# Kernel optimization log

Measured on AMD Instinct MI355X. Metric: run time of the kernel, lower is better.

Reference implementation:

```python
import jax, jax.numpy as jnp
import numpy as np

N = 4096
IN_DIM = 256
OUT_DIM = 256
NUM_HEADS = 4
HEAD_DIM = OUT_DIM // NUM_HEADS


def setup_inputs() -> dict:
    key = jax.random.key(0)
    ks = jax.random.split(key, 10)
    x = jax.random.normal(ks[0], (N, IN_DIM), dtype=jnp.float32)
    adj = jax.random.randint(ks[1], (N, N), 0, 2, dtype=jnp.int32)
    adj = jnp.maximum(adj, jnp.eye(N, dtype=jnp.int32))  # self-loops -> no empty rows
    s_in = 1.0 / np.sqrt(IN_DIM)
    s_out = 1.0 / np.sqrt(OUT_DIM)
    Wq = jax.random.uniform(ks[2], (IN_DIM, OUT_DIM), jnp.float32, -s_in, s_in)
    bq = jnp.zeros((OUT_DIM,), jnp.float32)
    Wk = jax.random.uniform(ks[3], (IN_DIM, OUT_DIM), jnp.float32, -s_in, s_in)
    bk = jnp.zeros((OUT_DIM,), jnp.float32)
    Wv = jax.random.uniform(ks[4], (IN_DIM, OUT_DIM), jnp.float32, -s_in, s_in)
    bv = jnp.zeros((OUT_DIM,), jnp.float32)
    Wo = jax.random.uniform(ks[5], (OUT_DIM, OUT_DIM), jnp.float32, -s_out, s_out)
    bo = jnp.zeros((OUT_DIM,), jnp.float32)
    gamma = jnp.ones((OUT_DIM,), jnp.float32)
    beta = jnp.zeros((OUT_DIM,), jnp.float32)
    return {"x": x, "adj": adj, "Wq": Wq, "bq": bq, "Wk": Wk, "bk": bk,
            "Wv": Wv, "bv": bv, "Wo": Wo, "bo": bo, "gamma": gamma, "beta": beta}


def layer_norm(h, gamma, beta, eps=1e-5):
    mu = jnp.mean(h, axis=-1, keepdims=True)
    var = jnp.mean(jnp.square(h - mu), axis=-1, keepdims=True)
    return (h - mu) * jax.lax.rsqrt(var + eps) * gamma + beta


def reference(x, adj, Wq, bq, Wk, bk, Wv, bv, Wo, bo, gamma, beta):
    n = x.shape[0]
    q_proj = x @ Wq + bq                       # (N, out_dim), reused for residual
    Q = q_proj.reshape(n, NUM_HEADS, HEAD_DIM)
    K = (x @ Wk + bk).reshape(n, NUM_HEADS, HEAD_DIM)
    V = (x @ Wv + bv).reshape(n, NUM_HEADS, HEAD_DIM)
    scores = jnp.einsum('nhd,mhd->nmh', Q, K) / np.sqrt(HEAD_DIM)
    scores = jnp.where(adj[:, :, None] == 0, -jnp.inf, scores)
    attn = jax.nn.softmax(scores, axis=1)      # softmax over neighbor axis m
    out = jnp.einsum('nmh,mhd->nhd', attn, V).reshape(n, OUT_DIM)
    out = out @ Wo + bo
    return layer_norm(out + q_proj, gamma, beta)
```

## Files before the change

### kernel.cpp

```cpp
#include <hip/hip_runtime.h>
#include <math.h>

#define NN 4096
#define DIM 256
#define NHEADS 4
#define HDIM 64

typedef short bf16x8 __attribute__((ext_vector_type(8)));
typedef float f32x4  __attribute__((ext_vector_type(4)));

__device__ __forceinline__ unsigned short f2bf(float f) {
    unsigned int u = __float_as_uint(f);
    u += 0x7fffu + ((u >> 16) & 1u);
    return (unsigned short)(u >> 16);
}
__device__ __forceinline__ float bf2f(unsigned short h) {
    return __uint_as_float(((unsigned int)h) << 16);
}
__device__ __forceinline__ void async16(const void* g, void* l) {
    __builtin_amdgcn_global_load_lds(
        (const __attribute__((address_space(1))) unsigned int*)g,
        (__attribute__((address_space(3))) unsigned int*)l, 16, 0, 0);
}

__global__ __launch_bounds__(256)
void prep_kernel(const float* __restrict__ W0, const float* __restrict__ W1,
                 const float* __restrict__ W2, const float* __restrict__ W3,
                 unsigned short* __restrict__ T0, unsigned short* __restrict__ T1,
                 unsigned short* __restrict__ T2, unsigned short* __restrict__ T3)
{
    __shared__ unsigned short Ts[64][65];
    const int b = blockIdx.x, t = threadIdx.x;
    const int mat = b >> 4, tile = b & 15;
    const int r0 = (tile >> 2) * 64, c0 = (tile & 3) * 64;
    const float* W = (mat == 0) ? W0 : (mat == 1) ? W1 : (mat == 2) ? W2 : W3;
    unsigned short* T = (mat == 0) ? T0 : (mat == 1) ? T1 : (mat == 2) ? T2 : T3;
    {
        int r = t >> 2, c4 = (t & 3) * 16;
        #pragma unroll
        for (int j = 0; j < 4; ++j) {
            float4 v = *reinterpret_cast<const float4*>(W + (size_t)(r0 + r) * DIM + c0 + c4 + j * 4);
            Ts[c4 + j * 4 + 0][r] = f2bf(v.x);
            Ts[c4 + j * 4 + 1][r] = f2bf(v.y);
            Ts[c4 + j * 4 + 2][r] = f2bf(v.z);
            Ts[c4 + j * 4 + 3][r] = f2bf(v.w);
        }
    }
    __syncthreads();
    {
        int d = t >> 2, k4 = (t & 3) * 16;
        #pragma unroll
        for (int j = 0; j < 4; ++j) {
            ushort4 u;
            u.x = Ts[d][k4 + j * 4 + 0];
            u.y = Ts[d][k4 + j * 4 + 1];
            u.z = Ts[d][k4 + j * 4 + 2];
            u.w = Ts[d][k4 + j * 4 + 3];
            *reinterpret_cast<ushort4*>(T + (size_t)(c0 + d) * DIM + r0 + k4 + j * 4) = u;
        }
    }
}

__global__ __launch_bounds__(256)
void qkv_mask(const float* __restrict__ x,
              const unsigned short* __restrict__ WqT, const unsigned short* __restrict__ WkT,
              const unsigned short* __restrict__ WvT,
              const float* __restrict__ bq, const float* __restrict__ bk, const float* __restrict__ bv,
              unsigned short* __restrict__ Qo, unsigned short* __restrict__ Ko,
              unsigned short* __restrict__ VTo,
              const int* __restrict__ adj, unsigned long long* __restrict__ maskT)
{
    const int b = blockIdx.x, t = threadIdx.x, w = t >> 6, l = t & 63;

    if (b >= 384) {
        const int ww = (b - 384) * 4 + w;
        for (int idx = ww; idx < 65536; idx += 8192) {
            const int row = idx >> 4, st = idx & 15;
            const int* ap = adj + (size_t)row * NN + st * 256 + l;
            const int a0 = ap[0];
            const int a1 = ap[64];
            const int a2 = ap[128];
            const int a3 = ap[192];
            unsigned long long b0 = __ballot(a0 != 0);
            unsigned long long b1 = __ballot(a1 != 0);
            unsigned long long b2 = __ballot(a2 != 0);
            unsigned long long b3 = __ballot(a3 != 0);
            if (l < 4) {
                unsigned long long bb = (l == 0) ? b0 : (l == 1) ? b1 : (l == 2) ? b2 : b3;
                maskT[(size_t)row * 64 + st * 4 + l] = bb;
            }
        }
        return;
    }

    const int l15 = l & 15, lg = l >> 4;
    const int which = b >> 7, xb = b & 127;
    const int row0 = xb * 32 + (w >> 1) * 16;
    const int col0 = (w & 1) * 128;
    const unsigned short* WT; const float* bias;
    if (which == 0)      { WT = WqT; bias = bq; }
    else if (which == 1) { WT = WkT; bias = bk; }
    else                 { WT = WvT; bias = bv; }

    f32x4 acc[8] = {};
    for (int k0 = 0; k0 < DIM; k0 += 32) {
        const float* xp = x + (size_t)(row0 + l15) * DIM + k0 + lg * 8;
        float4 x0 = *reinterpret_cast<const float4*>(xp);
        float4 x1 = *reinterpret_cast<const float4*>(xp + 4);
        union { unsigned u[4]; bf16x8 v; } xa;
        asm("v_cvt_pk_bf16_f32 %0, %1, %2" : "=v"(xa.u[0]) : "v"(x0.x), "v"(x0.y));
        asm("v_cvt_pk_bf16_f32 %0, %1, %2" : "=v"(xa.u[1]) : "v"(x0.z), "v"(x0.w));
        asm("v_cvt_pk_bf16_f32 %0, %1, %2" : "=v"(xa.u[2]) : "v"(x1.x), "v"(x1.y));
        asm("v_cvt_pk_bf16_f32 %0, %1, %2" : "=v"(xa.u[3]) : "v"(x1.z), "v"(x1.w));
        #pragma unroll
        for (int nt = 0; nt < 8; ++nt) {
            bf16x8 wb = *(const bf16x8*)(WT + (size_t)(col0 + nt * 16 + l15) * DIM + k0 + lg * 8);
            acc[nt] = __builtin_amdgcn_mfma_f32_16x16x32_bf16(xa.v, wb, acc[nt], 0, 0, 0);
        }
    }
    #pragma unroll
    for (int nt = 0; nt < 8; ++nt) {
        int col = col0 + nt * 16 + l15;
        float bb = bias[col];
        #pragma unroll
        for (int r = 0; r < 4; ++r) {
            int row = row0 + lg * 4 + r;
            float ov = acc[nt][r] + bb;
            if (which == 1) ov *= 0.18033688f;
            unsigned short val = f2bf(ov);
            if (which == 2) {
                int rb = row & 63;
                int vnt = rb >> 4, vlg = (rb >> 2) & 3, vr = rb & 3;
                int pos = ((vnt & 1) << 5) | (vlg << 3) | ((vnt >> 1) << 2) | vr;
                VTo[(size_t)col * NN + ((row & ~63) | pos)] = val;
            } else if (which == 0) Qo[(size_t)row * DIM + col] = val;
            else                   Ko[(size_t)row * DIM + col] = val;
        }
    }
}

template<int NTILES>
__global__ __launch_bounds__(256, 8)
void attn_mfma(const unsigned short* __restrict__ Qb, const unsigned short* __restrict__ Kb,
               const unsigned short* __restrict__ VT, const unsigned long long* __restrict__ maskT,
               unsigned short* __restrict__ Opart, float* __restrict__ lpart)
{
    constexpr int NSTR = NTILES / 4;
    __shared__ unsigned short Kt[2][64][64];
    __shared__ unsigned short Vt[2][64][64];

    const int t = threadIdx.x, w = t >> 6, l = t & 63, l15 = l & 15, lg = l >> 4;
    const int bid = blockIdx.x;
    const int slice = (bid & 7) + 8 * (bid >> 9);
    const int qb    = (bid >> 3) & 63;
    const int h  = slice & 3;
    const int sp = slice >> 2;
    const int n0 = qb * 64;
    const int kv_base = sp * NTILES * 64;
    const int qrow = n0 + w * 16;

    const unsigned short* qp = Qb + (size_t)(qrow + l15) * DIM + h * HDIM + lg * 8;
    const bf16x8 qa0 = *(const bf16x8*)(qp);
    const bf16x8 qa1 = *(const bf16x8*)(qp + 32);

    const unsigned long long* mbase = maskT + (size_t)(qrow + l15) * 64 + (kv_base >> 6);

    const int srow  = w * 16 + (l >> 3);
    const int sunit = (l & 7) ^ (srow & 7);
    const unsigned short* kS = Kb + (size_t)(kv_base + srow) * DIM + h * HDIM + sunit * 8;
    const unsigned short* vS = VT + (size_t)(h * HDIM + srow) * NN + kv_base + sunit * 8;

    const int xr  = l15 & 7;
    const int ko0 = (lg ^ xr) << 4;
    const int ko1 = ((4 + lg) ^ xr) << 4;

    const short onev = (l15 == 0) ? (short)0x3F80 : (short)0;
    const bf16x8 onesb = {onev, onev, onev, onev, onev, onev, onev, onev};

    f32x4 oa[4] = {};
    f32x4 os = {};

    {
        unsigned short* kd = &Kt[0][w * 16][0];
        unsigned short* vd = &Vt[0][w * 16][0];
        async16(kS, kd); async16(kS + 8 * DIM, kd + 8 * 64);
        async16(vS, vd); async16(vS + 8 * NN,  vd + 8 * 64);
    }

    #pragma unroll 1
    for (int st = 0; st < NSTR; ++st) {
        const ulonglong4 m4 = *reinterpret_cast<const ulonglong4*>(mbase + st * 4);

        #pragma unroll
        for (int m = 0; m < 4; ++m) {
            const int tl = st * 4 + m;
            asm volatile("s_waitcnt vmcnt(0)" ::: "memory");
            __builtin_amdgcn_s_barrier();
            __builtin_amdgcn_sched_barrier(0);

            if (tl + 1 < NTILES) {
                const int bb = (tl + 1) & 1;
                unsigned short* kd = &Kt[bb][w * 16][0];
                unsigned short* vd = &Vt[bb][w * 16][0];
                const unsigned short* ks = kS + (size_t)(tl + 1) * 64 * DIM;
                const unsigned short* vs = vS + (tl + 1) * 64;
                async16(ks, kd); async16(ks + 8 * DIM, kd + 8 * 64);
                async16(vs, vd); async16(vs + 8 * NN,  vd + 8 * 64);
            }

            const int cb = tl & 1;
            const char* kbase = (const char*)&Kt[cb][0][0] + l15 * 128;
            const char* vbase = (const char*)&Vt[cb][0][0] + l15 * 128;

            f32x4 sa[4] = {};
            __builtin_amdgcn_s_setprio(1);
            #pragma unroll
            for (int nt = 0; nt < 4; ++nt) {
                bf16x8 kb0 = *(const bf16x8*)(kbase + nt * 2048 + ko0);
                bf16x8 kb1 = *(const bf16x8*)(kbase + nt * 2048 + ko1);
                sa[nt] = __builtin_amdgcn_mfma_f32_16x16x32_bf16(kb0, qa0, sa[nt], 0, 0, 0);
                sa[nt] = __builtin_amdgcn_mfma_f32_16x16x32_bf16(kb1, qa1, sa[nt], 0, 0, 0);
            }
            __builtin_amdgcn_s_setprio(0);

            const unsigned long long w64 =
                (m == 0) ? m4.x : (m == 1) ? m4.y : (m == 2) ? m4.z : m4.w;
            const unsigned long long sh = w64 >> (lg * 4);
            const unsigned shlo = (unsigned)sh, shhi = (unsigned)(sh >> 32);
            float p[4][4];
            #pragma unroll
            for (int nt = 0; nt < 4; ++nt) {
                #pragma unroll
                for (int r = 0; r < 4; ++r) {
                    const int bitpos = nt * 16 + r;
                    const unsigned word = (bitpos < 32) ? shlo : shhi;
                    const unsigned bit = (word >> (bitpos & 31)) & 1u;
                    p[nt][r] = exp2f(bit ? sa[nt][r] : -INFINITY);
                }
            }
            union { unsigned u[4]; bf16x8 v; } a0, a1;
            asm("v_cvt_pk_bf16_f32 %0, %1, %2" : "=v"(a0.u[0]) : "v"(p[0][0]), "v"(p[0][1]));
            asm("v_cvt_pk_bf16_f32 %0, %1, %2" : "=v"(a0.u[1]) : "v"(p[0][2]), "v"(p[0][3]));
            asm("v_cvt_pk_bf16_f32 %0, %1, %2" : "=v"(a0.u[2]) : "v"(p[2][0]), "v"(p[2][1]));
            asm("v_cvt_pk_bf16_f32 %0, %1, %2" : "=v"(a0.u[3]) : "v"(p[2][2]), "v"(p[2][3]));
            asm("v_cvt_pk_bf16_f32 %0, %1, %2" : "=v"(a1.u[0]) : "v"(p[1][0]), "v"(p[1][1]));
            asm("v_cvt_pk_bf16_f32 %0, %1, %2" : "=v"(a1.u[1]) : "v"(p[1][2]), "v"(p[1][3]));
            asm("v_cvt_pk_bf16_f32 %0, %1, %2" : "=v"(a1.u[2]) : "v"(p[3][0]), "v"(p[3][1]));
            asm("v_cvt_pk_bf16_f32 %0, %1, %2" : "=v"(a1.u[3]) : "v"(p[3][2]), "v"(p[3][3]));
            const bf16x8 pa0 = a0.v;
            const bf16x8 pa1 = a1.v;

            __builtin_amdgcn_s_setprio(1);
            #pragma unroll
            for (int nt = 0; nt < 4; ++nt) {
                bf16x8 vb0 = *(const bf16x8*)(vbase + nt * 2048 + ko0);
                bf16x8 vb1 = *(const bf16x8*)(vbase + nt * 2048 + ko1);
                oa[nt] = __builtin_amdgcn_mfma_f32_16x16x32_bf16(pa0, vb0, oa[nt], 0, 0, 0);
                oa[nt] = __builtin_amdgcn_mfma_f32_16x16x32_bf16(pa1, vb1, oa[nt], 0, 0, 0);
            }
            os = __builtin_amdgcn_mfma_f32_16x16x32_bf16(pa0, onesb, os, 0, 0, 0);
            os = __builtin_amdgcn_mfma_f32_16x16x32_bf16(pa1, onesb, os, 0, 0, 0);
            __builtin_amdgcn_s_setprio(0);
        }
    }

    #pragma unroll
    for (int r = 0; r < 4; ++r) {
        const int qr = qrow + lg * 4 + r;
        #pragma unroll
        for (int nt = 0; nt < 4; ++nt)
            Opart[((size_t)sp * NN + qr) * DIM + h * HDIM + nt * 16 + l15] = f2bf(oa[nt][r]);
        if (l15 == 0)
            lpart[((size_t)sp * NN + qr) * NHEADS + h] = os[r];
    }
}

__global__ __launch_bounds__(256)
void combine_kernel(const unsigned short* __restrict__ Opart, const float* __restrict__ lpart,
                    unsigned short* __restrict__ AOb, int S)
{
    const int tid = blockIdx.x * blockDim.x + threadIdx.x;
    const int q  = tid >> 6;
    const int d  = (tid & 63) * 4;
    const int h  = d >> 6;
    float o0 = 0.f, o1 = 0.f, o2 = 0.f, o3 = 0.f, lsum = 0.f;
    for (int s = 0; s < S; ++s) {
        ushort4 u = *reinterpret_cast<const ushort4*>(Opart + ((size_t)s * NN + q) * DIM + d);
        o0 += bf2f(u.x); o1 += bf2f(u.y); o2 += bf2f(u.z); o3 += bf2f(u.w);
        lsum += lpart[((size_t)s * NN + q) * NHEADS + h];
    }
    float inv = 1.f / lsum;
    ushort4 o;
    o.x = f2bf(o0 * inv); o.y = f2bf(o1 * inv); o.z = f2bf(o2 * inv); o.w = f2bf(o3 * inv);
    *reinterpret_cast<ushort4*>(AOb + (size_t)q * DIM + d) = o;
}

__global__ __launch_bounds__(256)
void out_ln(const unsigned short* __restrict__ Ab, const unsigned short* __restrict__ WoT,
            const float* __restrict__ bo, const unsigned short* __restrict__ Rb,
            const float* __restrict__ gamma, const float* __restrict__ beta,
            float* __restrict__ out)
{
    __shared__ float redsum[4][16];
    __shared__ float redsq[4][16];
    const int t = threadIdx.x, w = t >> 6, l = t & 63, l15 = l & 15, lg = l >> 4;
    const int row0 = blockIdx.x * 16;
    const int col0 = w * 64;

    f32x4 acc[4] = {};
    for (int k0 = 0; k0 < DIM; k0 += 32) {
        bf16x8 xa = *(const bf16x8*)(Ab + (size_t)(row0 + l15) * DIM + k0 + lg * 8);
        #pragma unroll
        for (int nt = 0; nt < 4; ++nt) {
            bf16x8 wb = *(const bf16x8*)(WoT + (size_t)(col0 + nt * 16 + l15) * DIM + k0 + lg * 8);
            acc[nt] = __builtin_amdgcn_mfma_f32_16x16x32_bf16(xa, wb, acc[nt], 0, 0, 0);
        }
    }

    float psum[4] = {0, 0, 0, 0}, psq[4] = {0, 0, 0, 0};
    #pragma unroll
    for (int nt = 0; nt < 4; ++nt) {
        int col = col0 + nt * 16 + l15;
        float bb = bo[col];
        #pragma unroll
        for (int r = 0; r < 4; ++r) {
            int row = row0 + lg * 4 + r;
            float xv = acc[nt][r] + bb + bf2f(Rb[(size_t)row * DIM + col]);
            acc[nt][r] = xv;
            psum[r] += xv; psq[r] += xv * xv;
        }
    }
    #pragma unroll
    for (int r = 0; r < 4; ++r) {
        float s = psum[r], q = psq[r];
        s += __shfl_xor(s, 1); q += __shfl_xor(q, 1);
        s += __shfl_xor(s, 2); q += __shfl_xor(q, 2);
        s += __shfl_xor(s, 4); q += __shfl_xor(q, 4);
        s += __shfl_xor(s, 8); q += __shfl_xor(q, 8);
        psum[r] = s; psq[r] = q;
    }
    if (l15 == 0) {
        #pragma unroll
        for (int r = 0; r < 4; ++r) {
            redsum[w][lg * 4 + r] = psum[r];
            redsq[w][lg * 4 + r]  = psq[r];
        }
    }
    __syncthreads();

    float msave[4], rsave[4];
    #pragma unroll
    for (int r = 0; r < 4; ++r) {
        int row = lg * 4 + r;
        float s = redsum[0][row] + redsum[1][row] + redsum[2][row] + redsum[3][row];
        float q = redsq[0][row] + redsq[1][row] + redsq[2][row] + redsq[3][row];
        float mean = s * (1.f / 256.f);
        float var  = q * (1.f / 256.f) - mean * mean;
        msave[r] = mean;
        rsave[r] = rsqrtf(var + 1e-5f);
    }
    #pragma unroll
    for (int nt = 0; nt < 4; ++nt) {
        int col = col0 + nt * 16 + l15;
        float g = gamma[col], bt = beta[col];
        #pragma unroll
        for (int r = 0; r < 4; ++r) {
            int row = row0 + lg * 4 + r;
            out[(size_t)row * DIM + col] = (acc[nt][r] - msave[r]) * rsave[r] * g + bt;
        }
    }
}

extern "C" void kernel_launch(void* const* d_in, const int* in_sizes, int n_in,
                              void* d_out, int out_size, void* d_ws, size_t ws_size,
                              hipStream_t stream) {
    const float* x     = (const float*)d_in[0];
    const int*   adj   = (const int*)  d_in[1];
    const float* Wq    = (const float*)d_in[2];
    const float* bq    = (const float*)d_in[3];
    const float* Wk    = (const float*)d_in[4];
    const float* bk    = (const float*)d_in[5];
    const float* Wv    = (const float*)d_in[6];
    const float* bv    = (const float*)d_in[7];
    const float* Wo    = (const float*)d_in[8];
    const float* bo    = (const float*)d_in[9];
    const float* gamma = (const float*)d_in[10];
    const float* beta  = (const float*)d_in[11];
    float* out = (float*)d_out;

    char* ws = (char*)d_ws;
    const size_t MB = 1u << 20;
    unsigned short*     Qb    = (unsigned short*)(ws + 0 * MB);
    unsigned short*     Kb    = (unsigned short*)(ws + 2 * MB);
    unsigned short*     VT    = (unsigned short*)(ws + 4 * MB);
    unsigned long long* maskT = (unsigned long long*)(ws + 6 * MB);
    unsigned short*     WqT   = (unsigned short*)(ws + 8 * MB);
    unsigned short*     WkT   = (unsigned short*)(ws + 8 * MB + 128 * 1024);
    unsigned short*     WvT   = (unsigned short*)(ws + 8 * MB + 256 * 1024);
    unsigned short*     WoT   = (unsigned short*)(ws + 8 * MB + 384 * 1024);
    unsigned short*     AOb   = (unsigned short*)(ws + 8 * MB + 512 * 1024);
    float*              lpart = (float*)(ws + 10 * MB + 512 * 1024);
    unsigned short*     Opart = (unsigned short*)(ws + 11 * MB);

    const int S = (ws_size >= 27 * MB) ? 8 : 4;

    prep_kernel<<<64, 256, 0, stream>>>(Wq, Wk, Wv, Wo, WqT, WkT, WvT, WoT);

    qkv_mask<<<384 + 2048, 256, 0, stream>>>(
        x, WqT, WkT, WvT, bq, bk, bv, Qb, Kb, VT, adj, maskT);

    if (S == 8)
        attn_mfma<8><<<2048, 256, 0, stream>>>(Qb, Kb, VT, maskT, Opart, lpart);
    else
        attn_mfma<16><<<1024, 256, 0, stream>>>(Qb, Kb, VT, maskT, Opart, lpart);

    combine_kernel<<<NN * DIM / 4 / 256, 256, 0, stream>>>(Opart, lpart, AOb, S);

    out_ln<<<NN / 16, 256, 0, stream>>>(AOb, WoT, bo, Qb, gamma, beta, out);
}
```

Measured before the change: 86.50 us.

## Process 32 query rows per wave in attention to reuse K/V fragments

```diff
diff --git a/kernel.cpp b/kernel.cpp
--- a/kernel.cpp
+++ b/kernel.cpp
@@ -140,7 +140,7 @@
 }
 
 template<int NTILES>
-__global__ __launch_bounds__(256, 8)
+__global__ __launch_bounds__(256, 4)
 void attn_mfma(const unsigned short* __restrict__ Qb, const unsigned short* __restrict__ Kb,
                const unsigned short* __restrict__ VT, const unsigned long long* __restrict__ maskT,
                unsigned short* __restrict__ Opart, float* __restrict__ lpart)
@@ -151,19 +151,24 @@
 
     const int t = threadIdx.x, w = t >> 6, l = t & 63, l15 = l & 15, lg = l >> 4;
     const int bid = blockIdx.x;
-    const int slice = (bid & 7) + 8 * (bid >> 9);
-    const int qb    = (bid >> 3) & 63;
+    const int slice = (bid & 7) + 8 * (bid >> 8);
+    const int qb    = (bid >> 3) & 31;
     const int h  = slice & 3;
     const int sp = slice >> 2;
-    const int n0 = qb * 64;
+    const int n0 = qb * 128;
     const int kv_base = sp * NTILES * 64;
-    const int qrow = n0 + w * 16;
-
-    const unsigned short* qp = Qb + (size_t)(qrow + l15) * DIM + h * HDIM + lg * 8;
-    const bf16x8 qa0 = *(const bf16x8*)(qp);
-    const bf16x8 qa1 = *(const bf16x8*)(qp + 32);
-
-    const unsigned long long* mbase = maskT + (size_t)(qrow + l15) * 64 + (kv_base >> 6);
+    const int qrow = n0 + w * 32;
+
+    bf16x8 qa[2][2];
+    #pragma unroll
+    for (int sub = 0; sub < 2; ++sub) {
+        const unsigned short* qp = Qb + (size_t)(qrow + sub * 16 + l15) * DIM + h * HDIM + lg * 8;
+        qa[sub][0] = *(const bf16x8*)(qp);
+        qa[sub][1] = *(const bf16x8*)(qp + 32);
+    }
+
+    const unsigned long long* mbase0 = maskT + (size_t)(qrow + l15) * 64 + (kv_base >> 6);
+    const unsigned long long* mbase1 = maskT + (size_t)(qrow + 16 + l15) * 64 + (kv_base >> 6);
 
     const int srow  = w * 16 + (l >> 3);
     const int sunit = (l & 7) ^ (srow & 7);
@@ -177,8 +182,8 @@
     const short onev = (l15 == 0) ? (short)0x3F80 : (short)0;
     const bf16x8 onesb = {onev, onev, onev, onev, onev, onev, onev, onev};
 
-    f32x4 oa[4] = {};
-    f32x4 os = {};
+    f32x4 oa[2][4] = {};
+    f32x4 os[2] = {};
 
     {
         unsigned short* kd = &Kt[0][w * 16][0];
@@ -189,7 +194,8 @@
 
     #pragma unroll 1
     for (int st = 0; st < NSTR; ++st) {
-        const ulonglong4 m4 = *reinterpret_cast<const ulonglong4*>(mbase + st * 4);
+        const ulonglong4 m40 = *reinterpret_cast<const ulonglong4*>(mbase0 + st * 4);
+        const ulonglong4 m41 = *reinterpret_cast<const ulonglong4*>(mbase1 + st * 4);
 
         #pragma unroll
         for (int m = 0; m < 4; ++m) {
@@ -212,66 +218,82 @@
             const char* kbase = (const char*)&Kt[cb][0][0] + l15 * 128;
             const char* vbase = (const char*)&Vt[cb][0][0] + l15 * 128;
 
-            f32x4 sa[4] = {};
+            f32x4 sa[2][4] = {};
             __builtin_amdgcn_s_setprio(1);
             #pragma unroll
             for (int nt = 0; nt < 4; ++nt) {
                 bf16x8 kb0 = *(const bf16x8*)(kbase + nt * 2048 + ko0);
                 bf16x8 kb1 = *(const bf16x8*)(kbase + nt * 2048 + ko1);
-                sa[nt] = __builtin_amdgcn_mfma_f32_16x16x32_bf16(kb0, qa0, sa[nt], 0, 0, 0);
-                sa[nt] = __builtin_amdgcn_mfma_f32_16x16x32_bf16(kb1, qa1, sa[nt], 0, 0, 0);
+                sa[0][nt] = __builtin_amdgcn_mfma_f32_16x16x32_bf16(kb0, qa[0][0], sa[0][nt], 0, 0, 0);
+                sa[0][nt] = __builtin_amdgcn_mfma_f32_16x16x32_bf16(kb1, qa[0][1], sa[0][nt], 0, 0, 0);
+                sa[1][nt] = __builtin_amdgcn_mfma_f32_16x16x32_bf16(kb0, qa[1][0], sa[1][nt], 0, 0, 0);
+                sa[1][nt] = __builtin_amdgcn_mfma_f32_16x16x32_bf16(kb1, qa[1][1], sa[1][nt], 0, 0, 0);
             }
             __builtin_amdgcn_s_setprio(0);
 
-            const unsigned long long w64 =
-                (m == 0) ? m4.x : (m == 1) ? m4.y : (m == 2) ? m4.z : m4.w;
-            const unsigned long long sh = w64 >> (lg * 4);
-            const unsigned shlo = (unsigned)sh, shhi = (unsigned)(sh >> 32);
-            float p[4][4];
+            bf16x8 vb0[4], vb1[4];
             #pragma unroll
             for (int nt = 0; nt < 4; ++nt) {
+                vb0[nt] = *(const bf16x8*)(vbase + nt * 2048 + ko0);
+                vb1[nt] = *(const bf16x8*)(vbase + nt * 2048 + ko1);
+            }
+
+            #pragma unroll
+            for (int sub = 0; sub < 2; ++sub) {
+                const ulonglong4& m4 = sub ? m41 : m40;
+                const unsigned long long w64 =
+                    (m == 0) ? m4.x : (m == 1) ? m4.y : (m == 2) ? m4.z : m4.w;
+                const unsigned long long shq = w64 >> (lg * 4);
+                const unsigned shlo = (unsigned)shq, shhi = (unsigned)(shq >> 32);
+                float p[4][4];
                 #pragma unroll
-                for (int r = 0; r < 4; ++r) {
-                    const int bitpos = nt * 16 + r;
-                    const unsigned word = (bitpos < 32) ? shlo : shhi;
-                    const unsigned bit = (word >> (bitpos & 31)) & 1u;
-                    p[nt][r] = exp2f(bit ? sa[nt][r] : -INFINITY);
+                for (int nt = 0; nt < 4; ++nt) {
+                    #pragma unroll
+                    for (int r = 0; r < 4; ++r) {
+                        const int bitpos = nt * 16 + r;
+                        const unsigned word = (bitpos < 32) ? shlo : shhi;
+                        const unsigned bit = (word >> (bitpos & 31)) & 1u;
+                        p[nt][r] = exp2f(bit ? sa[sub][nt][r] : -INFINITY);
+                    }
                 }
+                union { unsigned u[4]; bf16x8 v; } a0, a1;
+                asm("v_cvt_pk_bf16_f32 %0, %1, %2" : "=v"(a0.u[0]) : "v"(p[0][0]), "v"(p[0][1]));
+                asm("v_cvt_pk_bf16_f32 %0, %1, %2" : "=v"(a0.u[1]) : "v"(p[0][2]), "v"(p[0][3]));
+                asm("v_cvt_pk_bf16_f32 %0, %1, %2" : "=v"(a0.u[2]) : "v"(p[2][0]), "v"(p[2][1]));
+                asm("v_cvt_pk_bf16_f32 %0, %1, %2" : "=v"(a0.u[3]) : "v"(p[2][2]), "v"(p[2][3]));
+                asm("v_cvt_pk_bf16_f32 %0, %1, %2" : "=v"(a1.u[0]) : "v"(p[1][0]), "v"(p[1][1]));
+                asm("v_cvt_pk_bf16_f32 %0, %1, %2" : "=v"(a1.u[1]) : "v"(p[1][2]), "v"(p[1][3]));
+                asm("v_cvt_pk_bf16_f32 %0, %1, %2" : "=v"(a1.u[2]) : "v"(p[3][0]), "v"(p[3][1]));
+                asm("v_cvt_pk_bf16_f32 %0, %1, %2" : "=v"(a1.u[3]) : "v"(p[3][2]), "v"(p[3][3]));
+                const bf16x8 pa0 = a0.v;
+                const bf16x8 pa1 = a1.v;
+
+                __builtin_amdgcn_s_setprio(1);
+                #pragma unroll
+                for (int nt = 0; nt < 4; ++nt) {
+                    oa[sub][nt] = __builtin_amdgcn_mfma_f32_16x16x32_bf16(pa0, vb0[nt], oa[sub][nt], 0, 0, 0);
+                    oa[sub][nt] = __builtin_amdgcn_mfma_f32_16x16x32_bf16(pa1, vb1[nt], oa[sub][nt], 0, 0, 0);
+                }
+                os[sub] = __builtin_amdgcn_mfma_f32_16x16x32_bf16(pa0, onesb, os[sub], 0, 0, 0);
+                os[sub] = __builtin_amdgcn_mfma_f32_16x16x32_bf16(pa1, onesb, os[sub], 0, 0, 0);
+                __builtin_amdgcn_s_setprio(0);
             }
-            union { unsigned u[4]; bf16x8 v; } a0, a1;
-            asm("v_cvt_pk_bf16_f32 %0, %1, %2" : "=v"(a0.u[0]) : "v"(p[0][0]), "v"(p[0][1]));
-            asm("v_cvt_pk_bf16_f32 %0, %1, %2" : "=v"(a0.u[1]) : "v"(p[0][2]), "v"(p[0][3]));
-            asm("v_cvt_pk_bf16_f32 %0, %1, %2" : "=v"(a0.u[2]) : "v"(p[2][0]), "v"(p[2][1]));
-            asm("v_cvt_pk_bf16_f32 %0, %1, %2" : "=v"(a0.u[3]) : "v"(p[2][2]), "v"(p[2][3]));
-            asm("v_cvt_pk_bf16_f32 %0, %1, %2" : "=v"(a1.u[0]) : "v"(p[1][0]), "v"(p[1][1]));
-            asm("v_cvt_pk_bf16_f32 %0, %1, %2" : "=v"(a1.u[1]) : "v"(p[1][2]), "v"(p[1][3]));
-            asm("v_cvt_pk_bf16_f32 %0, %1, %2" : "=v"(a1.u[2]) : "v"(p[3][0]), "v"(p[3][1]));
-            asm("v_cvt_pk_bf16_f32 %0, %1, %2" : "=v"(a1.u[3]) : "v"(p[3][2]), "v"(p[3][3]));
-            const bf16x8 pa0 = a0.v;
-            const bf16x8 pa1 = a1.v;
-
-            __builtin_amdgcn_s_setprio(1);
+
+            __builtin_amdgcn_sched_barrier(0);
+        }
+    }
+
+    #pragma unroll
+    for (int sub = 0; sub < 2; ++sub) {
+        #pragma unroll
+        for (int r = 0; r < 4; ++r) {
+            const int qr = qrow + sub * 16 + lg * 4 + r;
             #pragma unroll
-            for (int nt = 0; nt < 4; ++nt) {
-                bf16x8 vb0 = *(const bf16x8*)(vbase + nt * 2048 + ko0);
-                bf16x8 vb1 = *(const bf16x8*)(vbase + nt * 2048 + ko1);
-                oa[nt] = __builtin_amdgcn_mfma_f32_16x16x32_bf16(pa0, vb0, oa[nt], 0, 0, 0);
-                oa[nt] = __builtin_amdgcn_mfma_f32_16x16x32_bf16(pa1, vb1, oa[nt], 0, 0, 0);
-            }
-            os = __builtin_amdgcn_mfma_f32_16x16x32_bf16(pa0, onesb, os, 0, 0, 0);
-            os = __builtin_amdgcn_mfma_f32_16x16x32_bf16(pa1, onesb, os, 0, 0, 0);
-            __builtin_amdgcn_s_setprio(0);
-        }
-    }
-
-    #pragma unroll
-    for (int r = 0; r < 4; ++r) {
-        const int qr = qrow + lg * 4 + r;
-        #pragma unroll
-        for (int nt = 0; nt < 4; ++nt)
-            Opart[((size_t)sp * NN + qr) * DIM + h * HDIM + nt * 16 + l15] = f2bf(oa[nt][r]);
-        if (l15 == 0)
-            lpart[((size_t)sp * NN + qr) * NHEADS + h] = os[r];
+            for (int nt = 0; nt < 4; ++nt)
+                Opart[((size_t)sp * NN + qr) * DIM + h * HDIM + nt * 16 + l15] = f2bf(oa[sub][nt][r]);
+            if (l15 == 0)
+                lpart[((size_t)sp * NN + qr) * NHEADS + h] = os[sub][r];
+        }
     }
 }
 
@@ -410,9 +432,9 @@
         x, WqT, WkT, WvT, bq, bk, bv, Qb, Kb, VT, adj, maskT);
 
     if (S == 8)
-        attn_mfma<8><<<2048, 256, 0, stream>>>(Qb, Kb, VT, maskT, Opart, lpart);
+        attn_mfma<8><<<1024, 256, 0, stream>>>(Qb, Kb, VT, maskT, Opart, lpart);
     else
-        attn_mfma<16><<<1024, 256, 0, stream>>>(Qb, Kb, VT, maskT, Opart, lpart);
+        attn_mfma<16><<<512, 256, 0, stream>>>(Qb, Kb, VT, maskT, Opart, lpart);
 
     combine_kernel<<<NN * DIM / 4 / 256, 256, 0, stream>>>(Opart, lpart, AOb, S);
 
```

After: 118.3 us. 1.37x slower.
